# Optimization experiments

Measured on AMD Instinct MI355X. Metric: run time of the kernel, lower is better.

The kernel has to match this reference:

```python
import jax, jax.numpy as jnp
import numpy as np

TOPK = 8
N_EXPERTS = 64
ROUTE_SCALE = 1.0


def setup_inputs() -> dict:
    key = jax.random.key(0)
    k1, k2 = jax.random.split(key)
    x = jax.random.normal(k1, (16, 256, 64, 64), dtype=jnp.float32)
    gate_w = jax.random.normal(k2, (64, 256, 3, 3), dtype=jnp.float32) * 0.02  # [E, C, kh, kw]
    bias = jnp.zeros((64,), dtype=jnp.float32)  # load-balancing bias buffer
    return {"x": x, "gate_w": gate_w, "bias": bias}


def reference(x, gate_w, bias):
    # 3x3 conv, stride 1, pad 1 (SAME), no conv bias -> expert logits [B, E, H, W]
    logits = jax.lax.conv_general_dilated(
        x, gate_w, window_strides=(1, 1), padding="SAME",
        dimension_numbers=("NCHW", "OIHW", "NCHW"))
    scores = jax.nn.sigmoid(logits)                 # [B, E, H, W]
    s = jnp.moveaxis(scores, 1, -1)                 # [B, H, W, E]
    biased = s + bias                               # bias broadcast over experts
    _, idx = jax.lax.top_k(biased, TOPK)            # [B, H, W, K] (topk on biased scores)
    w = jnp.take_along_axis(s, idx, axis=-1)        # gather UNbiased scores
    w = jax.nn.softmax(w, axis=-1) * ROUTE_SCALE    # softmax over the K selected experts
    weights = jnp.moveaxis(w, -1, 1)                # [B, K, H, W] to match torch layout
    indices = jnp.moveaxis(idx, -1, 1)              # [B, K, H, W]
    counts = jnp.zeros((N_EXPERTS,), jnp.int32).at[idx.ravel()].add(1)  # bincount
    return weights, indices, counts
```

## Files before the change

### kernel.cpp

```cpp
#include <hip/hip_runtime.h>


typedef _Float16 half8 __attribute__((ext_vector_type(8)));
typedef __attribute__((ext_vector_type(4))) float f32x4;

#define LOG2E 1.44269504f

__device__ __forceinline__ unsigned short f2h_bits(float f) {
    _Float16 h = (_Float16)f;
    unsigned short b;
    __builtin_memcpy(&b, &h, 2);
    return b;
}

constexpr int WB_U4 = 8 * 9 * 4 * 64;
constexpr size_t XT_BYTES = (size_t)16 * 66 * 8 * 66 * 32 * 2;
constexpr size_t WS_NEED  = XT_BYTES + (size_t)WB_U4 * 16 + 262144;

#define GLOAD16(gp, lp)                                                    \
    __builtin_amdgcn_global_load_lds(                                      \
        (const __attribute__((address_space(1))) void*)(gp),               \
        (__attribute__((address_space(3))) void*)(lp), 16, 0, 0)


constexpr int NB_INT = 4096, NB_BOR = 130, NB_WB = 72;
constexpr int PREP_GRID = NB_INT + NB_BOR + NB_WB;

__global__ __launch_bounds__(256) void prep_all2(
    const float* __restrict__ x, const float* __restrict__ gw,
    _Float16* __restrict__ xT, unsigned short* __restrict__ wB,
    float* __restrict__ out) {
    const int blk = blockIdx.x, tid = threadIdx.x;
    if (blk < NB_INT) {
        int gid = blk * 256 + tid;
        int w = gid & 63, c16 = (gid >> 6) & 15, h = (gid >> 10) & 63, b = gid >> 16;
        int c0 = c16 * 16;
        const float* src = x + ((b * 256 + c0) * 64 + h) * 64 + w;
        float v[16];
#pragma unroll
        for (int j = 0; j < 16; ++j) v[j] = src[j * 4096];
        uint4 p0, p1;
        p0.x = (unsigned)f2h_bits(v[0])  | ((unsigned)f2h_bits(v[1])  << 16);
        p0.y = (unsigned)f2h_bits(v[2])  | ((unsigned)f2h_bits(v[3])  << 16);
        p0.z = (unsigned)f2h_bits(v[4])  | ((unsigned)f2h_bits(v[5])  << 16);
        p0.w = (unsigned)f2h_bits(v[6])  | ((unsigned)f2h_bits(v[7])  << 16);
        p1.x = (unsigned)f2h_bits(v[8])  | ((unsigned)f2h_bits(v[9])  << 16);
        p1.y = (unsigned)f2h_bits(v[10]) | ((unsigned)f2h_bits(v[11]) << 16);
        p1.z = (unsigned)f2h_bits(v[12]) | ((unsigned)f2h_bits(v[13]) << 16);
        p1.w = (unsigned)f2h_bits(v[14]) | ((unsigned)f2h_bits(v[15]) << 16);
        int q = c16 >> 1;
        size_t idx = ((((size_t)b * 66 + h + 1) * 8 + q) * 66 + (w + 1)) * 32
                     + (c16 & 1) * 16;
        uint4* dst = (uint4*)(xT + idx);
        dst[0] = p0; dst[1] = p1;
    } else if (blk < NB_INT + NB_BOR) {
        int t = (blk - NB_INT) * 256 + tid;
        int q = t & 7, site = t >> 3;
        int sb = site / 260, s = site - sb * 260;
        int hp, wp;
        if (s < 132) { hp = (s >= 66) ? 65 : 0; wp = (s >= 66) ? (s - 66) : s; }
        else         { int s2 = s - 132; hp = 1 + (s2 >> 1); wp = (s2 & 1) * 65; }
        uint4 z = {0u, 0u, 0u, 0u};
        size_t idx = ((((size_t)sb * 66 + hp) * 8 + q) * 66 + wp) * 32;
        uint4* dst = (uint4*)(xT + idx);
#pragma unroll
        for (int k = 0; k < 4; ++k) dst[k] = z;
    } else {
        int wblk = blk - (NB_INT + NB_BOR);
        if (wblk == 0 && tid < 64) out[1048576 + tid] = 0.f;
        int g = wblk * 256 + tid;
        int lane = g & 63;
        int nt   = (g >> 6) & 3;
        int rest = g >> 8;
        int t = rest % 9, q = rest / 9;
        int e  = nt * 16 + (lane & 15);
        int c0 = q * 32 + (lane >> 4) * 8;
        unsigned short o[8];
#pragma unroll
        for (int j = 0; j < 8; ++j)
            o[j] = f2h_bits(gw[(e * 256 + c0 + j) * 9 + t]);
        uint4 pk;
        pk.x = (unsigned)o[0] | ((unsigned)o[1] << 16);
        pk.y = (unsigned)o[2] | ((unsigned)o[3] << 16);
        pk.z = (unsigned)o[4] | ((unsigned)o[5] << 16);
        pk.w = (unsigned)o[6] | ((unsigned)o[7] << 16);
        ((uint4*)wB)[g] = pk;
    }
}

constexpr int SSTR = 68;
constexpr int HALFB = 12672;

__global__ __launch_bounds__(256, 4) void gate_main4(
    const _Float16* __restrict__ xT, const float* __restrict__ bias,
    const unsigned short* __restrict__ wB, float* __restrict__ out) {
    __shared__ uint4 smem4[2 * HALFB / 16];
    __shared__ float bias_s[64];
    __shared__ int   hist[64];
    char* smem = (char*)smem4;

    const int tid  = threadIdx.x;
    const int lane = tid & 63;
    const int rw   = tid >> 6;
    const int blk  = blockIdx.x;
    const int b    = blk & 15;
    const int r    = blk >> 4;

    if (tid < 64) { bias_s[tid] = bias[tid]; hist[tid] = 0; }

    const int ph = rw >> 1, eh = rw & 1;

    const _Float16* srcP[4];
    int ldsOff[4];
    const bool act3 = (tid < 24);
#pragma unroll
    for (int i = 0; i < 4; ++i) {
        int T = tid + i * 256;
        if (T >= 792) T = 0;
        int seg = T / 264, o = T - seg * 264;
        srcP[i]  = xT + ((size_t)(b * 66 + r + seg) * 8) * 2112 + o * 8;
        ldsOff[i] = T * 16;
    }
    auto STAGE = [&](int q, int halfB) {
#pragma unroll
        for (int i = 0; i < 3; ++i)
            GLOAD16(srcP[i] + q * 2112, smem + ldsOff[i] + halfB);
        if (act3)
            GLOAD16(srcP[3] + q * 2112, smem + ldsOff[3] + halfB);
    };

    const char* aP0 = smem + ((ph * 32 + (lane & 15)) * 64 + (lane >> 4) * 16);
    half8 Aa[3][2];
    uint4 Bb[6][2];
    f32x4 acc[2][2];
#pragma unroll
    for (int mt = 0; mt < 2; ++mt)
#pragma unroll
        for (int nt = 0; nt < 2; ++nt) acc[mt][nt] = (f32x4){0.f, 0.f, 0.f, 0.f};

    auto LDA = [&](int kh, int kw, int slot, int HB) {
        Aa[slot][0] = *(const half8*)(aP0 + HB + kh * 4224 + kw * 64);
        Aa[slot][1] = *(const half8*)(aP0 + HB + kh * 4224 + kw * 64 + 1024);
    };
    const char* bP = (const char*)wB + eh * 2048 + lane * 16;
    auto LDB = [&](int slot) {
        Bb[slot][0] = *(const uint4*)bP;
        Bb[slot][1] = *(const uint4*)(bP + 1024);
        bP += 4096;
    };
    auto MT = [&](int as, int bs) {
#pragma unroll
        for (int nt = 0; nt < 2; ++nt) {
            half8 bfr;
            __builtin_memcpy(&bfr, &Bb[bs][nt], 16);
#pragma unroll
            for (int m = 0; m < 2; ++m)
                acc[m][nt] = __builtin_amdgcn_mfma_f32_16x16x32_f16(
                    Aa[as][m], bfr, acc[m][nt], 0, 0, 0);
        }
    };
    auto SB = []() { __builtin_amdgcn_sched_barrier(0); };

    STAGE(0, 0);
    LDB(0); LDB(1); LDB(2); LDB(3); LDB(4); LDB(5);
    SB();
    asm volatile("s_waitcnt vmcnt(12)" ::: "memory");
    __builtin_amdgcn_s_barrier();
    SB();

#pragma unroll 1
    for (int i = 0; i < 4; ++i) {
        STAGE(2 * i + 1, HALFB);
        LDA(0, 0, 0, 0); LDA(0, 1, 1, 0); LDA(0, 2, 2, 0);
        SB();
        MT(0, 0); LDA(1, 0, 0, 0); LDB(0); SB();
        MT(1, 1); LDA(1, 1, 1, 0); LDB(1); SB();
        MT(2, 2); LDA(1, 2, 2, 0); LDB(2); SB();
        MT(0, 3); LDA(2, 0, 0, 0); LDB(3); SB();
        MT(1, 4); LDA(2, 1, 1, 0); LDB(4); SB();
        MT(2, 5); LDA(2, 2, 2, 0); LDB(5); SB();
        MT(0, 0); LDB(0); SB();
        MT(1, 1); LDB(1); SB();
        MT(2, 2); LDB(2); SB();
        SB();
        asm volatile("s_waitcnt vmcnt(18) lgkmcnt(0)" ::: "memory");
        __builtin_amdgcn_s_barrier();
        SB();
        if (i < 3) STAGE(2 * i + 2, 0);
        LDA(0, 0, 0, HALFB); LDA(0, 1, 1, HALFB); LDA(0, 2, 2, HALFB);
        SB();
        MT(0, 3); LDA(1, 0, 0, HALFB); LDB(3); SB();
        MT(1, 4); LDA(1, 1, 1, HALFB); LDB(4); SB();
        MT(2, 5); LDA(1, 2, 2, HALFB); LDB(5); SB();
        MT(0, 0); LDA(2, 0, 0, HALFB); LDB(0); SB();
        MT(1, 1); LDA(2, 1, 1, HALFB); LDB(1); SB();
        MT(2, 2); LDA(2, 2, 2, HALFB); LDB(2); SB();
        MT(0, 3); LDB(3); SB();
        MT(1, 4); LDB(4); SB();
        MT(2, 5); LDB(5); SB();
        if (i < 3) {
            SB();
            asm volatile("s_waitcnt vmcnt(18) lgkmcnt(0)" ::: "memory");
            __builtin_amdgcn_s_barrier();
            SB();
        }
    }
    __syncthreads();

    float* scf = (float*)smem4;
#pragma unroll
    for (int mt = 0; mt < 2; ++mt)
#pragma unroll
        for (int nt = 0; nt < 2; ++nt)
#pragma unroll
            for (int rr = 0; rr < 4; ++rr) {
                float v = acc[mt][nt][rr];
                float s = 1.f / (1.f + __builtin_amdgcn_exp2f(-v * LOG2E));
                int p = ph * 32 + mt * 16 + ((lane >> 4) << 2) + rr;
                int e = eh * 32 + nt * 16 + (lane & 15);
                scf[p * SSTR + e] = s;
            }
    __syncthreads();

    if (tid < 64) {
        const float* row = scf + tid * SSTR;
        float tv[8];
        int   ti[8];
#pragma unroll
        for (int k = 0; k < 8; ++k) { tv[k] = -3.0e38f; ti[k] = 0; }
#pragma unroll
        for (int j4 = 0; j4 < 16; ++j4) {
            f32x4 blkv = *(const f32x4*)(row + j4 * 4);
#pragma unroll
            for (int j = 0; j < 4; ++j) {
                int   e  = j4 * 4 + j;
                float bs = blkv[j] + bias_s[e];
                if (bs > tv[7]) {
                    tv[7] = bs; ti[7] = e;
#pragma unroll
                    for (int k = 7; k > 0; --k) {
                        float fa = tv[k - 1], fb = tv[k];
                        int   ia = ti[k - 1], ib = ti[k];
                        bool  sw = fb > fa;
                        tv[k - 1] = sw ? fb : fa; tv[k] = sw ? fa : fb;
                        ti[k - 1] = sw ? ib : ia; ti[k] = sw ? ia : ib;
                    }
                }
            }
        }
        float u[8], mx = -3.0e38f;
#pragma unroll
        for (int k = 0; k < 8; ++k) { u[k] = tv[k] - bias_s[ti[k]]; mx = fmaxf(mx, u[k]); }
        float ex[8], sum = 0.f;
#pragma unroll
        for (int k = 0; k < 8; ++k) { ex[k] = __builtin_amdgcn_exp2f((u[k] - mx) * LOG2E); sum += ex[k]; }
        float inv = 1.f / sum;

        int obase = b * 32768 + r * 64 + tid;
#pragma unroll
        for (int k = 0; k < 8; ++k) {
            out[obase + k * 4096]          = ex[k] * inv;
            out[524288 + obase + k * 4096] = (float)ti[k];
            atomicAdd(&hist[ti[k]], 1);
        }
    }
    __syncthreads();
    if (tid < 64) atomicAdd(out + 1048576 + tid, (float)hist[tid]);
}


__global__ __launch_bounds__(256) void gate_prep(const float* __restrict__ gw,
                                                 unsigned short* __restrict__ wB,
                                                 float* __restrict__ out) {
    int g = blockIdx.x * 256 + threadIdx.x;
    if (blockIdx.x == 0 && threadIdx.x < 64) out[1048576 + threadIdx.x] = 0.f;
    if (g >= WB_U4) return;
    int lane = g & 63;
    int nt   = (g >> 6) & 3;
    int rest = g >> 8;
    int t = rest % 9, q = rest / 9;
    int e  = nt * 16 + (lane & 15);
    int c0 = q * 32 + (lane >> 4) * 8;
    unsigned short o[8];
#pragma unroll
    for (int j = 0; j < 8; ++j)
        o[j] = f2h_bits(gw[(e * 256 + c0 + j) * 9 + t]);
    uint4 pk;
    pk.x = (unsigned)o[0] | ((unsigned)o[1] << 16);
    pk.y = (unsigned)o[2] | ((unsigned)o[3] << 16);
    pk.z = (unsigned)o[4] | ((unsigned)o[5] << 16);
    pk.w = (unsigned)o[6] | ((unsigned)o[7] << 16);
    ((uint4*)wB)[g] = pk;
}

constexpr int CSTR = 40;
constexpr int SLAB = 3 * 66 * CSTR;

__global__ __launch_bounds__(256, 4) void gate_main_fb(
    const float* __restrict__ x, const float* __restrict__ bias,
    const unsigned short* __restrict__ wB, float* __restrict__ out) {
    __shared__ unsigned short xs[2 * SLAB];
    __shared__ float bias_s[64];
    __shared__ int   hist[64];

    const int tid  = threadIdx.x;
    const int lane = tid & 63;
    const int rw   = tid >> 6;
    const int blk  = blockIdx.x;
    const int b    = blk & 15;
    const int r    = blk >> 4;

    if (tid < 64) { bias_s[tid] = bias[tid]; hist[tid] = 0; }
    {
        uint4 z = {0u, 0u, 0u, 0u};
        uint4* p = (uint4*)xs;
#pragma unroll
        for (int i = 0; i < 8; ++i) {
            int idx = tid + i * 256;
            if (idx < 2 * SLAB / 8) p[idx] = z;
        }
    }

    bool tOk[4];
    int  tSrc[4], tDst[4];
#pragma unroll
    for (int i = 0; i < 4; ++i) {
        int T = tid + i * 256;
        bool ex = (T < 792);
        int chh = T / 198, s = T - chh * 198;
        int row2 = s / 66, wp = s - row2 * 66;
        int gr = r - 1 + row2, gwc = wp - 1;
        tOk[i]  = ex && (gr >= 0) && (gr < 64) && (gwc >= 0) && (gwc < 64);
        tSrc[i] = ((b * 256 + chh * 8) * 64 + gr) * 64 + gwc;
        tDst[i] = (row2 * 66 + wp) * CSTR + chh * 8;
    }

    float tb[4][8];
    auto issueT = [&](int i, int dq) {
        if (tOk[i]) {
            const float* p = x + tSrc[i] + dq * 131072;
#pragma unroll
            for (int u = 0; u < 8; ++u) tb[i][u] = p[u * 4096];
        }
    };
    auto commitT = [&](int i, unsigned short* dst) {
        if (tOk[i]) {
            uint4 pk;
            pk.x = (unsigned)f2h_bits(tb[i][0]) | ((unsigned)f2h_bits(tb[i][1]) << 16);
            pk.y = (unsigned)f2h_bits(tb[i][2]) | ((unsigned)f2h_bits(tb[i][3]) << 16);
            pk.z = (unsigned)f2h_bits(tb[i][4]) | ((unsigned)f2h_bits(tb[i][5]) << 16);
            pk.w = (unsigned)f2h_bits(tb[i][6]) | ((unsigned)f2h_bits(tb[i][7]) << 16);
            *(uint4*)(dst + tDst[i]) = pk;
        }
    };

    const int ph = rw >> 1, eh = rw & 1;
    half8 Aa[3][2];
    uint4 Bb[3][2];
    auto prefA = [&](const unsigned short* buf, int t, int slot) {
        const int kh = t / 3, kw = t % 3;
        const unsigned short* abase =
            buf + (kh * 66 + ph * 32 + (lane & 15) + kw) * CSTR + (lane >> 4) * 8;
#pragma unroll
        for (int mt = 0; mt < 2; ++mt)
            Aa[slot][mt] = *(const half8*)(abase + mt * 16 * CSTR);
    };
    auto prefB = [&](int T9, int slot) {
        const uint4* bp = (const uint4*)wB + (T9 * 4 + eh * 2) * 64 + lane;
#pragma unroll
        for (int nt = 0; nt < 2; ++nt) Bb[slot][nt] = bp[nt * 64];
    };

    f32x4 acc[2][2];
#pragma unroll
    for (int mt = 0; mt < 2; ++mt)
#pragma unroll
        for (int nt = 0; nt < 2; ++nt) acc[mt][nt] = (f32x4){0.f, 0.f, 0.f, 0.f};

    auto mfma_tap = [&](int slot) {
#pragma unroll
        for (int nt = 0; nt < 2; ++nt) {
            half8 bfr;
            __builtin_memcpy(&bfr, &Bb[slot][nt], 16);
#pragma unroll
            for (int mt = 0; mt < 2; ++mt)
                acc[mt][nt] = __builtin_amdgcn_mfma_f32_16x16x32_f16(
                    Aa[slot][mt], bfr, acc[mt][nt], 0, 0, 0);
        }
    };

    __syncthreads();
    issueT(0, 0); issueT(1, 0); issueT(2, 0); issueT(3, 0);
    commitT(0, xs); commitT(1, xs); commitT(2, xs); commitT(3, xs);
    issueT(0, 1); issueT(1, 1); issueT(2, 1); issueT(3, 1);
    prefB(0, 0); prefB(1, 1); prefB(2, 2);
    __syncthreads();

#pragma unroll 1
    for (int q = 0; q < 8; ++q) {
        const unsigned short* cur = xs + (q & 1) * SLAB;
        unsigned short*       nxt = xs + ((q + 1) & 1) * SLAB;
        const int  T0  = q * 9;
        const bool cmt = (q < 7);
        const bool iss = (q < 6);

        prefA(cur, 0, 0); prefA(cur, 1, 1);
        mfma_tap(0); prefB(T0 + 3, 0); prefA(cur, 2, 2);
        mfma_tap(1); prefB(T0 + 4, 1); prefA(cur, 3, 0);
        if (cmt) { commitT(0, nxt); commitT(1, nxt); }
        mfma_tap(2); prefB(T0 + 5, 2); prefA(cur, 4, 1);
        mfma_tap(0); prefB(T0 + 6, 0); prefA(cur, 5, 2);
        if (cmt) { commitT(2, nxt); commitT(3, nxt); }
        mfma_tap(1); prefB(T0 + 7, 1); prefA(cur, 6, 0);
        mfma_tap(2); prefB(T0 + 8, 2); prefA(cur, 7, 1);
        __builtin_amdgcn_sched_barrier(0);
        if (iss) { issueT(0, q + 2); issueT(1, q + 2); issueT(2, q + 2); issueT(3, q + 2); }
        __builtin_amdgcn_sched_barrier(0);
        mfma_tap(0); if (cmt) prefB(T0 + 9, 0);  prefA(cur, 8, 2);
        mfma_tap(1); if (cmt) prefB(T0 + 10, 1);
        mfma_tap(2); if (cmt) prefB(T0 + 11, 2);
        __syncthreads();
    }

    float* scf2 = (float*)xs;
#pragma unroll
    for (int mt = 0; mt < 2; ++mt)
#pragma unroll
        for (int nt = 0; nt < 2; ++nt)
#pragma unroll
            for (int rr = 0; rr < 4; ++rr) {
                float v = acc[mt][nt][rr];
                float s = 1.f / (1.f + __builtin_amdgcn_exp2f(-v * LOG2E));
                int p = ph * 32 + mt * 16 + ((lane >> 4) << 2) + rr;
                int e = eh * 32 + nt * 16 + (lane & 15);
                scf2[p * SSTR + e] = s;
            }
    __syncthreads();

    if (tid < 64) {
        const float* row = scf2 + tid * SSTR;
        float tv[8];
        int   ti[8];
#pragma unroll
        for (int k = 0; k < 8; ++k) { tv[k] = -3.0e38f; ti[k] = 0; }
#pragma unroll
        for (int j4 = 0; j4 < 16; ++j4) {
            f32x4 blkv = *(const f32x4*)(row + j4 * 4);
#pragma unroll
            for (int j = 0; j < 4; ++j) {
                int   e  = j4 * 4 + j;
                float bs = blkv[j] + bias_s[e];
                if (bs > tv[7]) {
                    tv[7] = bs; ti[7] = e;
#pragma unroll
                    for (int k = 7; k > 0; --k) {
                        float fa = tv[k - 1], fb = tv[k];
                        int   ia = ti[k - 1], ib = ti[k];
                        bool  sw = fb > fa;
                        tv[k - 1] = sw ? fb : fa; tv[k] = sw ? fa : fb;
                        ti[k - 1] = sw ? ib : ia; ti[k] = sw ? ia : ib;
                    }
                }
            }
        }
        float u[8], mx = -3.0e38f;
#pragma unroll
        for (int k = 0; k < 8; ++k) { u[k] = tv[k] - bias_s[ti[k]]; mx = fmaxf(mx, u[k]); }
        float ex[8], sum = 0.f;
#pragma unroll
        for (int k = 0; k < 8; ++k) { ex[k] = __builtin_amdgcn_exp2f((u[k] - mx) * LOG2E); sum += ex[k]; }
        float inv = 1.f / sum;

        int obase = b * 32768 + r * 64 + tid;
#pragma unroll
        for (int k = 0; k < 8; ++k) {
            out[obase + k * 4096]          = ex[k] * inv;
            out[524288 + obase + k * 4096] = (float)ti[k];
            atomicAdd(&hist[ti[k]], 1);
        }
    }
    __syncthreads();
    if (tid < 64) atomicAdd(out + 1048576 + tid, (float)hist[tid]);
}

extern "C" void kernel_launch(void* const* d_in, const int* in_sizes, int n_in,
                              void* d_out, int out_size, void* d_ws, size_t ws_size,
                              hipStream_t stream) {
    const float* x    = (const float*)d_in[0];
    const float* gw   = (const float*)d_in[1];
    const float* bias = (const float*)d_in[2];
    float* out = (float*)d_out;

    if (ws_size >= WS_NEED) {
        _Float16* xT = (_Float16*)d_ws;
        unsigned short* wB = (unsigned short*)((char*)d_ws + XT_BYTES);
        prep_all2<<<PREP_GRID, 256, 0, stream>>>(x, gw, xT, wB, out);
        gate_main4<<<1024, 256, 0, stream>>>(xT, bias, wB, out);
    } else {
        unsigned short* wB = (unsigned short*)d_ws;
        gate_prep<<<72, 256, 0, stream>>>(gw, wB, out);
        gate_main_fb<<<1024, 256, 0, stream>>>(x, bias, wB, out);
    }
}
```

Before: 155.0 us.

## XOR-swizzle LDS A-tile layout and widen prep transpose to 32 channels

The main kernel now applies an XOR swizzle to the 16-byte chunk order when staging the padded input into LDS, with matching per-kw base pointers for the A-fragment reads. This is meant to remove LDS bank conflicts on the MFMA operand loads. The prep kernel now has each thread convert 32 channels and write a full 64-byte site, which halves the prep grid and makes the stores wider. The cost is more registers per prep thread and extra address arithmetic, and the swizzled reads must exactly match the staging permutation to stay correct.

```diff
diff --git a/kernel.cpp b/kernel.cpp
--- a/kernel.cpp
+++ b/kernel.cpp
@@ -23,36 +23,32 @@
         (__attribute__((address_space(3))) void*)(lp), 16, 0, 0)
 
 
-constexpr int NB_INT = 4096, NB_BOR = 130, NB_WB = 72;
+constexpr int NB_INT = 2048, NB_BOR = 130, NB_WB = 72;
 constexpr int PREP_GRID = NB_INT + NB_BOR + NB_WB;
 
-__global__ __launch_bounds__(256) void prep_all2(
+__global__ __launch_bounds__(256) void prep_all3(
     const float* __restrict__ x, const float* __restrict__ gw,
     _Float16* __restrict__ xT, unsigned short* __restrict__ wB,
     float* __restrict__ out) {
     const int blk = blockIdx.x, tid = threadIdx.x;
     if (blk < NB_INT) {
         int gid = blk * 256 + tid;
-        int w = gid & 63, c16 = (gid >> 6) & 15, h = (gid >> 10) & 63, b = gid >> 16;
-        int c0 = c16 * 16;
-        const float* src = x + ((b * 256 + c0) * 64 + h) * 64 + w;
-        float v[16];
-#pragma unroll
-        for (int j = 0; j < 16; ++j) v[j] = src[j * 4096];
-        uint4 p0, p1;
-        p0.x = (unsigned)f2h_bits(v[0])  | ((unsigned)f2h_bits(v[1])  << 16);
-        p0.y = (unsigned)f2h_bits(v[2])  | ((unsigned)f2h_bits(v[3])  << 16);
-        p0.z = (unsigned)f2h_bits(v[4])  | ((unsigned)f2h_bits(v[5])  << 16);
-        p0.w = (unsigned)f2h_bits(v[6])  | ((unsigned)f2h_bits(v[7])  << 16);
-        p1.x = (unsigned)f2h_bits(v[8])  | ((unsigned)f2h_bits(v[9])  << 16);
-        p1.y = (unsigned)f2h_bits(v[10]) | ((unsigned)f2h_bits(v[11]) << 16);
-        p1.z = (unsigned)f2h_bits(v[12]) | ((unsigned)f2h_bits(v[13]) << 16);
-        p1.w = (unsigned)f2h_bits(v[14]) | ((unsigned)f2h_bits(v[15]) << 16);
-        int q = c16 >> 1;
-        size_t idx = ((((size_t)b * 66 + h + 1) * 8 + q) * 66 + (w + 1)) * 32
-                     + (c16 & 1) * 16;
-        uint4* dst = (uint4*)(xT + idx);
-        dst[0] = p0; dst[1] = p1;
+        int w = gid & 63, q = (gid >> 6) & 7, h = (gid >> 9) & 63, b = gid >> 15;
+        const float* src = x + (((b * 256 + q * 32) * 64 + h) * 64 + w);
+        float v[32];
+#pragma unroll
+        for (int j = 0; j < 32; ++j) v[j] = src[j * 4096];
+        uint4 pk[4];
+#pragma unroll
+        for (int c8 = 0; c8 < 4; ++c8) {
+            pk[c8].x = (unsigned)f2h_bits(v[c8 * 8 + 0]) | ((unsigned)f2h_bits(v[c8 * 8 + 1]) << 16);
+            pk[c8].y = (unsigned)f2h_bits(v[c8 * 8 + 2]) | ((unsigned)f2h_bits(v[c8 * 8 + 3]) << 16);
+            pk[c8].z = (unsigned)f2h_bits(v[c8 * 8 + 4]) | ((unsigned)f2h_bits(v[c8 * 8 + 5]) << 16);
+            pk[c8].w = (unsigned)f2h_bits(v[c8 * 8 + 6]) | ((unsigned)f2h_bits(v[c8 * 8 + 7]) << 16);
+        }
+        size_t site = ((size_t)(b * 66 + h + 1) * 8 + q) * 66 + (w + 1);
+        uint4* dst = (uint4*)xT + site * 4;
+        dst[0] = pk[0]; dst[1] = pk[1]; dst[2] = pk[2]; dst[3] = pk[3];
     } else if (blk < NB_INT + NB_BOR) {
         int t = (blk - NB_INT) * 256 + tid;
         int q = t & 7, site = t >> 3;
@@ -118,7 +114,8 @@
         int T = tid + i * 256;
         if (T >= 792) T = 0;
         int seg = T / 264, o = T - seg * 264;
-        srcP[i]  = xT + ((size_t)(b * 66 + r + seg) * 8) * 2112 + o * 8;
+        int osrc = (o & ~3) | ((o & 3) ^ ((o >> 3) & 3));
+        srcP[i]  = xT + ((size_t)(b * 66 + r + seg) * 8) * 2112 + osrc * 8;
         ldsOff[i] = T * 16;
     }
     auto STAGE = [&](int q, int halfB) {
@@ -129,7 +126,15 @@
             GLOAD16(srcP[3] + q * 2112, smem + ldsOff[3] + halfB);
     };
 
-    const char* aP0 = smem + ((ph * 32 + (lane & 15)) * 64 + (lane >> 4) * 16);
+    const int wl = ph * 32 + (lane & 15);
+    const char* aB[3];
+#pragma unroll
+    for (int kw = 0; kw < 3; ++kw) {
+        int wp = wl + kw;
+        int c8 = (lane >> 4) ^ ((wp >> 1) & 3);
+        aB[kw] = smem + wp * 64 + c8 * 16;
+    }
+
     half8 Aa[3][2];
     uint4 Bb[6][2];
     f32x4 acc[2][2];
@@ -139,8 +144,8 @@
         for (int nt = 0; nt < 2; ++nt) acc[mt][nt] = (f32x4){0.f, 0.f, 0.f, 0.f};
 
     auto LDA = [&](int kh, int kw, int slot, int HB) {
-        Aa[slot][0] = *(const half8*)(aP0 + HB + kh * 4224 + kw * 64);
-        Aa[slot][1] = *(const half8*)(aP0 + HB + kh * 4224 + kw * 64 + 1024);
+        Aa[slot][0] = *(const half8*)(aB[kw] + HB + kh * 4224);
+        Aa[slot][1] = *(const half8*)(aB[kw] + HB + kh * 4224 + 1024);
     };
     const char* bP = (const char*)wB + eh * 2048 + lane * 16;
     auto LDB = [&](int slot) {
@@ -494,7 +499,7 @@
     if (ws_size >= WS_NEED) {
         _Float16* xT = (_Float16*)d_ws;
         unsigned short* wB = (unsigned short*)((char*)d_ws + XT_BYTES);
-        prep_all2<<<PREP_GRID, 256, 0, stream>>>(x, gw, xT, wB, out);
+        prep_all3<<<PREP_GRID, 256, 0, stream>>>(x, gw, xT, wB, out);
         gate_main4<<<1024, 256, 0, stream>>>(xT, bias, wB, out);
     } else {
         unsigned short* wB = (unsigned short*)d_ws;
```

Measured after the change: 158.8 us. +2.4%, slower.

## Split conv gate blocks into half-rows with swizzled LDS and rotated channel phases

Applied to the files above, without the earlier changes.

Replaces the 256-thread block per output row with two 128-thread blocks, each covering half a row (32 pixels) and all 64 experts, doubling the grid to 2048 blocks. Input staging now loads only the 34 needed columns into a smaller XOR-swizzled LDS tile to avoid bank conflicts. Each block starts its channel-chunk loop at a different phase so that concurrent blocks read different weight slices. The aim is better occupancy and load balance with less shared memory, at the cost of reloading the halo and weights per half-row.

```diff
diff --git a/kernel.cpp b/kernel.cpp
--- a/kernel.cpp
+++ b/kernel.cpp
@@ -88,48 +88,58 @@
     }
 }
 
-constexpr int SSTR = 68;
-constexpr int HALFB = 12672;
-
-__global__ __launch_bounds__(256, 4) void gate_main4(
+constexpr int SSTR6 = 68;
+constexpr int HALF6 = 8192;
+
+__global__ __launch_bounds__(128, 4) void gate_main6(
     const _Float16* __restrict__ xT, const float* __restrict__ bias,
     const unsigned short* __restrict__ wB, float* __restrict__ out) {
-    __shared__ uint4 smem4[2 * HALFB / 16];
+    __shared__ uint4 smem4[2 * HALF6 / 16];
     __shared__ float bias_s[64];
     __shared__ int   hist[64];
     char* smem = (char*)smem4;
 
     const int tid  = threadIdx.x;
     const int lane = tid & 63;
-    const int rw   = tid >> 6;
+    const int eh   = tid >> 6;
     const int blk  = blockIdx.x;
     const int b    = blk & 15;
-    const int r    = blk >> 4;
+    const int r    = (blk >> 4) & 63;
+    const int ph   = blk >> 10;
+    const int phase = (blk >> 8) & 7;
 
     if (tid < 64) { bias_s[tid] = bias[tid]; hist[tid] = 0; }
 
-    const int ph = rw >> 1, eh = rw & 1;
-
-    const _Float16* srcP[4];
-    int ldsOff[4];
-    const bool act3 = (tid < 24);
+    const _Float16* srcB[4];
+    int loff[4];
 #pragma unroll
     for (int i = 0; i < 4; ++i) {
-        int T = tid + i * 256;
-        if (T >= 792) T = 0;
-        int seg = T / 264, o = T - seg * 264;
-        srcP[i]  = xT + ((size_t)(b * 66 + r + seg) * 8) * 2112 + o * 8;
-        ldsOff[i] = T * 16;
-    }
-    auto STAGE = [&](int q, int halfB) {
-#pragma unroll
-        for (int i = 0; i < 3; ++i)
-            GLOAD16(srcP[i] + q * 2112, smem + ldsOff[i] + halfB);
-        if (act3)
-            GLOAD16(srcP[3] + q * 2112, smem + ldsOff[3] + halfB);
-    };
-
-    const char* aP0 = smem + ((ph * 32 + (lane & 15)) * 64 + (lane >> 4) * 16);
+        int T = tid + i * 128;
+        loff[i] = T * 16;
+        if (T < 408) {
+            int st = T >> 2, c8s = T & 3;
+            int seg = st / 34, s = st - seg * 34;
+            int c8 = c8s ^ ((s >> 1) & 3);
+            srcB[i] = xT + ((size_t)((b * 66 + r + seg) * 8)) * 2112
+                         + (ph * 32 + s) * 32 + c8 * 8;
+        } else {
+            srcB[i] = xT;
+        }
+    }
+    auto STAGE = [&](int q, int HB) {
+#pragma unroll
+        for (int i = 0; i < 4; ++i)
+            GLOAD16(srcB[i] + q * 2112, smem + loff[i] + HB);
+    };
+
+    const char* aB[3];
+#pragma unroll
+    for (int kw = 0; kw < 3; ++kw) {
+        int s  = (lane & 15) + kw;
+        int c8 = (lane >> 4) ^ ((s >> 1) & 3);
+        aB[kw] = smem + s * 64 + c8 * 16;
+    }
+
     half8 Aa[3][2];
     uint4 Bb[6][2];
     f32x4 acc[2][2];
@@ -139,14 +149,13 @@
         for (int nt = 0; nt < 2; ++nt) acc[mt][nt] = (f32x4){0.f, 0.f, 0.f, 0.f};
 
     auto LDA = [&](int kh, int kw, int slot, int HB) {
-        Aa[slot][0] = *(const half8*)(aP0 + HB + kh * 4224 + kw * 64);
-        Aa[slot][1] = *(const half8*)(aP0 + HB + kh * 4224 + kw * 64 + 1024);
-    };
-    const char* bP = (const char*)wB + eh * 2048 + lane * 16;
-    auto LDB = [&](int slot) {
-        Bb[slot][0] = *(const uint4*)bP;
-        Bb[slot][1] = *(const uint4*)(bP + 1024);
-        bP += 4096;
+        Aa[slot][0] = *(const half8*)(aB[kw] + HB + kh * 2176);
+        Aa[slot][1] = *(const half8*)(aB[kw] + HB + kh * 2176 + 1024);
+    };
+    const char* wBeh = (const char*)wB + eh * 2048 + lane * 16;
+    auto LDBo = [&](const char* p, int off, int slot) {
+        Bb[slot][0] = *(const uint4*)(p + off);
+        Bb[slot][1] = *(const uint4*)(p + off + 1024);
     };
     auto MT = [&](int as, int bs) {
 #pragma unroll
@@ -161,49 +170,56 @@
     };
     auto SB = []() { __builtin_amdgcn_sched_barrier(0); };
 
-    STAGE(0, 0);
-    LDB(0); LDB(1); LDB(2); LDB(3); LDB(4); LDB(5);
+    const char* p0 = wBeh + phase * 36864;
+    STAGE(phase, 0);
+    LDBo(p0, 0, 0); LDBo(p0, 4096, 1); LDBo(p0, 8192, 2);
+    LDBo(p0, 12288, 3); LDBo(p0, 16384, 4); LDBo(p0, 20480, 5);
     SB();
     asm volatile("s_waitcnt vmcnt(12)" ::: "memory");
     __builtin_amdgcn_s_barrier();
     SB();
+    const char* pC = p0 + 24576;
 
 #pragma unroll 1
-    for (int i = 0; i < 4; ++i) {
-        STAGE(2 * i + 1, HALFB);
-        LDA(0, 0, 0, 0); LDA(0, 1, 1, 0); LDA(0, 2, 2, 0);
-        SB();
-        MT(0, 0); LDA(1, 0, 0, 0); LDB(0); SB();
-        MT(1, 1); LDA(1, 1, 1, 0); LDB(1); SB();
-        MT(2, 2); LDA(1, 2, 2, 0); LDB(2); SB();
-        MT(0, 3); LDA(2, 0, 0, 0); LDB(3); SB();
-        MT(1, 4); LDA(2, 1, 1, 0); LDB(4); SB();
-        MT(2, 5); LDA(2, 2, 2, 0); LDB(5); SB();
-        MT(0, 0); LDB(0); SB();
-        MT(1, 1); LDB(1); SB();
-        MT(2, 2); LDB(2); SB();
+    for (int ii = 0; ii < 4; ++ii) {
+        int qn = (phase + 2 * ii + 1) & 7;
+        const char* pN = wBeh + qn * 36864;
+        STAGE(qn, HALF6);
+        LDA(0, 0, 0, 0); LDA(0, 1, 1, 0); LDA(0, 2, 2, 0); SB();
+        MT(0, 0); LDA(1, 0, 0, 0); LDBo(pC, 0, 0);     SB();
+        MT(1, 1); LDA(1, 1, 1, 0); LDBo(pC, 4096, 1);  SB();
+        MT(2, 2); LDA(1, 2, 2, 0); LDBo(pC, 8192, 2);  SB();
+        MT(0, 3); LDA(2, 0, 0, 0); LDBo(pN, 0, 3);     SB();
+        MT(1, 4); LDA(2, 1, 1, 0); LDBo(pN, 4096, 4);  SB();
+        MT(2, 5); LDA(2, 2, 2, 0); LDBo(pN, 8192, 5);  SB();
+        MT(0, 0); LDBo(pN, 12288, 0); SB();
+        MT(1, 1); LDBo(pN, 16384, 1); SB();
+        MT(2, 2); LDBo(pN, 20480, 2); SB();
         SB();
         asm volatile("s_waitcnt vmcnt(18) lgkmcnt(0)" ::: "memory");
         __builtin_amdgcn_s_barrier();
         SB();
-        if (i < 3) STAGE(2 * i + 2, 0);
-        LDA(0, 0, 0, HALFB); LDA(0, 1, 1, HALFB); LDA(0, 2, 2, HALFB);
-        SB();
-        MT(0, 3); LDA(1, 0, 0, HALFB); LDB(3); SB();
-        MT(1, 4); LDA(1, 1, 1, HALFB); LDB(4); SB();
-        MT(2, 5); LDA(1, 2, 2, HALFB); LDB(5); SB();
-        MT(0, 0); LDA(2, 0, 0, HALFB); LDB(0); SB();
-        MT(1, 1); LDA(2, 1, 1, HALFB); LDB(1); SB();
-        MT(2, 2); LDA(2, 2, 2, HALFB); LDB(2); SB();
-        MT(0, 3); LDB(3); SB();
-        MT(1, 4); LDB(4); SB();
-        MT(2, 5); LDB(5); SB();
-        if (i < 3) {
+        pC = pN + 24576;
+        int qn2 = (phase + 2 * ii + 2) & 7;
+        const char* pN2 = wBeh + qn2 * 36864;
+        if (ii < 3) STAGE(qn2, 0);
+        LDA(0, 0, 0, HALF6); LDA(0, 1, 1, HALF6); LDA(0, 2, 2, HALF6); SB();
+        MT(0, 3); LDA(1, 0, 0, HALF6); LDBo(pC, 0, 3);     SB();
+        MT(1, 4); LDA(1, 1, 1, HALF6); LDBo(pC, 4096, 4);  SB();
+        MT(2, 5); LDA(1, 2, 2, HALF6); LDBo(pC, 8192, 5);  SB();
+        MT(0, 0); LDA(2, 0, 0, HALF6); LDBo(pN2, 0, 0);    SB();
+        MT(1, 1); LDA(2, 1, 1, HALF6); LDBo(pN2, 4096, 1); SB();
+        MT(2, 2); LDA(2, 2, 2, HALF6); LDBo(pN2, 8192, 2); SB();
+        MT(0, 3); LDBo(pN2, 12288, 3); SB();
+        MT(1, 4); LDBo(pN2, 16384, 4); SB();
+        MT(2, 5); LDBo(pN2, 20480, 5); SB();
+        if (ii < 3) {
             SB();
             asm volatile("s_waitcnt vmcnt(18) lgkmcnt(0)" ::: "memory");
             __builtin_amdgcn_s_barrier();
             SB();
         }
+        pC = pN2 + 24576;
     }
     __syncthreads();
 
@@ -216,14 +232,14 @@
             for (int rr = 0; rr < 4; ++rr) {
                 float v = acc[mt][nt][rr];
                 float s = 1.f / (1.f + __builtin_amdgcn_exp2f(-v * LOG2E));
-                int p = ph * 32 + mt * 16 + ((lane >> 4) << 2) + rr;
+                int p = mt * 16 + ((lane >> 4) << 2) + rr;
                 int e = eh * 32 + nt * 16 + (lane & 15);
-                scf[p * SSTR + e] = s;
+                scf[p * SSTR6 + e] = s;
             }
     __syncthreads();
 
-    if (tid < 64) {
-        const float* row = scf + tid * SSTR;
+    if (tid < 32) {
+        const float* row = scf + tid * SSTR6;
         float tv[8];
         int   ti[8];
 #pragma unroll
@@ -256,7 +272,7 @@
         for (int k = 0; k < 8; ++k) { ex[k] = __builtin_amdgcn_exp2f((u[k] - mx) * LOG2E); sum += ex[k]; }
         float inv = 1.f / sum;
 
-        int obase = b * 32768 + r * 64 + tid;
+        int obase = b * 32768 + r * 64 + ph * 32 + tid;
 #pragma unroll
         for (int k = 0; k < 8; ++k) {
             out[obase + k * 4096]          = ex[k] * inv;
@@ -295,6 +311,7 @@
 
 constexpr int CSTR = 40;
 constexpr int SLAB = 3 * 66 * CSTR;
+constexpr int SSTR = 68;
 
 __global__ __launch_bounds__(256, 4) void gate_main_fb(
     const float* __restrict__ x, const float* __restrict__ bias,
@@ -495,7 +512,7 @@
         _Float16* xT = (_Float16*)d_ws;
         unsigned short* wB = (unsigned short*)((char*)d_ws + XT_BYTES);
         prep_all2<<<PREP_GRID, 256, 0, stream>>>(x, gw, xT, wB, out);
-        gate_main4<<<1024, 256, 0, stream>>>(xT, bias, wB, out);
+        gate_main6<<<2048, 128, 0, stream>>>(xT, bias, wB, out);
     } else {
         unsigned short* wB = (unsigned short*)d_ws;
         gate_prep<<<72, 256, 0, stream>>>(gw, wB, out);
```

After: 189.5 us. 1.22x slower.
